# Kernel optimization log

Hardware: AMD Instinct MI355X
Metric: run time of the kernel (lower is better)

The kernel has to match this reference:

```python
import jax, jax.numpy as jnp
import numpy as np

TOP_K = 2  # num_experts_per_tok


def setup_inputs() -> dict:
    key = jax.random.key(0)
    ks = jax.random.split(key, 5)
    B, T, D, E, F = 2, 2048, 1024, 8, 2048
    scale_d = 1.0 / np.sqrt(D)
    scale_f = 1.0 / np.sqrt(F)
    return {
        "x": jax.random.normal(ks[0], (B, T, D), jnp.float32),
        "kernel_router_DE": jax.random.normal(ks[1], (D, E), jnp.float32) * scale_d,
        "kernel_gating_EDF": jax.random.normal(ks[2], (E, D, F), jnp.float32) * scale_d,
        "kernel_up_EDF": jax.random.normal(ks[3], (E, D, F), jnp.float32) * scale_d,
        "kernel_down_EFD": jax.random.normal(ks[4], (E, F, D), jnp.float32) * scale_f,
    }


def reference(x, kernel_router_DE, kernel_gating_EDF, kernel_up_EDF, kernel_down_EFD):
    E = kernel_router_DE.shape[-1]
    x = x.astype(jnp.float32)

    # --- Router: logits -> softmax -> top_k -> renormalize with softmax ---
    router_logits_BTE = jnp.einsum('BTD,DE->BTE', x, kernel_router_DE)
    probs_BTE = jax.nn.softmax(router_logits_BTE.astype(jnp.float32), axis=-1)
    weights_BTX, indices_BTX = jax.lax.top_k(probs_BTE, TOP_K)
    norm_weights_BTX = jax.nn.softmax(weights_BTX, axis=-1)

    # --- Scatter top-k weights back to dense per-expert weights ---
    one_hot_BTXE = jax.nn.one_hot(indices_BTX, num_classes=E, dtype=jnp.float32)
    full_weights_BTE = jnp.sum(one_hot_BTXE * norm_weights_BTX[..., None], axis=2)

    # --- Dense all-expert MLP (gating * up -> down), weighted combine ---
    gating_BTEF = jnp.einsum('BTD,EDF->BTEF', x, kernel_gating_EDF)
    fuse_BTEF = jax.nn.silu(gating_BTEF) * jnp.einsum('BTD,EDF->BTEF', x, kernel_up_EDF)
    down_BTED = jnp.einsum('BTEF,EFD->BTED', fuse_BTEF, kernel_down_EFD)
    out_BTD = jnp.einsum('BTED,BTE->BTD', down_BTED, full_weights_BTE)
    return out_BTD.astype(jnp.float32)
```

## Files before the change

### kernel.cpp

```cpp
#include <hip/hip_runtime.h>
#include <cstdint>

#define N_TOK 4096
#define DIM   1024
#define NEXP  8
#define FDIM  2048

typedef _Float16 f16_t;
typedef _Float16 f16x8 __attribute__((ext_vector_type(8)));
typedef float    f32x4 __attribute__((ext_vector_type(4)));

__device__ inline unsigned packh(float a, float b) {
    union { f16_t h[2]; unsigned u; } p;
    p.h[0] = (f16_t)a; p.h[1] = (f16_t)b;
    return p.u;
}

__device__ inline void gl2lds16(const void* g, void* l) {
    __builtin_amdgcn_global_load_lds(
        (const __attribute__((address_space(1))) unsigned*)g,
        (__attribute__((address_space(3))) unsigned*)l, 16, 0, 0);
}

__global__ __launch_bounds__(256) void router_kernel(
    const float* __restrict__ x, const float* __restrict__ wr,
    float* __restrict__ topw, int* __restrict__ counts, int* __restrict__ bucket)
{
    __shared__ float r[NEXP][DIM];
    __shared__ int sIdx[32];
    int tid = threadIdx.x;
    for (int i = tid; i < DIM * NEXP / 4; i += 256) {
        float4 v = ((const float4*)wr)[i];
        int base = i * 4;
        r[(base + 0) & 7][(base + 0) >> 3] = v.x;
        r[(base + 1) & 7][(base + 1) >> 3] = v.y;
        r[(base + 2) & 7][(base + 2) >> 3] = v.z;
        r[(base + 3) & 7][(base + 3) >> 3] = v.w;
    }
    __syncthreads();
    int wave = tid >> 6, lane = tid & 63;
    int t0 = blockIdx.x * 16 + wave * 4;
    for (int tt = 0; tt < 4; ++tt) {
        int t = t0 + tt;
        float acc[NEXP];
#pragma unroll
        for (int e = 0; e < NEXP; e++) acc[e] = 0.f;
        const float* xr = x + (size_t)t * DIM;
#pragma unroll
        for (int k = 0; k < DIM / 64; k++) {
            int d = lane + k * 64;
            float xv = xr[d];
#pragma unroll
            for (int e = 0; e < NEXP; e++) acc[e] += xv * r[e][d];
        }
#pragma unroll
        for (int e = 0; e < NEXP; e++) {
#pragma unroll
            for (int off = 32; off > 0; off >>= 1)
                acc[e] += __shfl_xor(acc[e], off, 64);
        }
        if (lane == 0) {
            float mx = acc[0];
#pragma unroll
            for (int e = 1; e < NEXP; e++) mx = fmaxf(mx, acc[e]);
            float p[NEXP]; float s = 0.f;
#pragma unroll
            for (int e = 0; e < NEXP; e++) { p[e] = expf(acc[e] - mx); s += p[e]; }
            float inv = 1.f / s;
#pragma unroll
            for (int e = 0; e < NEXP; e++) p[e] *= inv;
            int i1 = 0; float p1 = p[0];
#pragma unroll
            for (int e = 1; e < NEXP; e++) if (p[e] > p1) { p1 = p[e]; i1 = e; }
            int i2 = -1; float p2 = -1.f;
#pragma unroll
            for (int e = 0; e < NEXP; e++) if (e != i1 && p[e] > p2) { p2 = p[e]; i2 = e; }
            float e2 = expf(p2 - p1);
            float w1 = 1.f / (1.f + e2);
            topw[t * 2 + 0] = w1;
            topw[t * 2 + 1] = e2 * w1;
            int j = (wave * 4 + tt) * 2;
            sIdx[j + 0] = i1;
            sIdx[j + 1] = i2;
        }
    }
    __syncthreads();
    if (tid < NEXP) {
        int cnt = 0;
#pragma unroll
        for (int j = 0; j < 32; j++) cnt += (sIdx[j] == tid) ? 1 : 0;
        if (cnt > 0) {
            int pos = atomicAdd(&counts[tid * 32], cnt);
#pragma unroll
            for (int j = 0; j < 32; j++)
                if (sIdx[j] == tid)
                    bucket[tid * N_TOK + pos++] = (blockIdx.x * 16 + (j >> 1)) * 2 + (j & 1);
        }
    }
}

__global__ __launch_bounds__(256) void xcast_kernel(const float* __restrict__ x, f16_t* __restrict__ xf)
{
    int i = blockIdx.x * 256 + threadIdx.x;
    float4 a = ((const float4*)x)[2 * i];
    float4 b = ((const float4*)x)[2 * i + 1];
    union { f16_t h[8]; uint4 u; } p;
    p.h[0] = (f16_t)a.x; p.h[1] = (f16_t)a.y; p.h[2] = (f16_t)a.z; p.h[3] = (f16_t)a.w;
    p.h[4] = (f16_t)b.x; p.h[5] = (f16_t)b.y; p.h[6] = (f16_t)b.z; p.h[7] = (f16_t)b.w;
    ((uint4*)xf)[i] = p.u;
}

__global__ __launch_bounds__(256) void transpose_cvt(
    const float* __restrict__ inA, const float* __restrict__ inB,
    f16_t* __restrict__ outA, f16_t* __restrict__ outB,
    int R, int C, int tiles_r, int nA)
{
    __shared__ unsigned sP[64][68];
    int m = blockIdx.y;
    const float* in; f16_t* out;
    if (m < nA) { in = inA + (size_t)m * DIM * FDIM; out = outA + (size_t)m * DIM * FDIM; }
    else        { in = inB + (size_t)(m - nA) * DIM * FDIM; out = outB + (size_t)(m - nA) * DIM * FDIM; }
    int tix = blockIdx.x;
    int rb = (tix % tiles_r) * 128;
    int cb = (tix / tiles_r) * 64;
    int t = threadIdx.x;
    int dp = t >> 2;
    int fc = (t & 3) * 16;
    const float* r0 = in + (size_t)(rb + 2 * dp) * C + cb + fc;
    const float* r1 = r0 + C;
#pragma unroll
    for (int j = 0; j < 16; j += 4) {
        float4 a = *(const float4*)(r0 + j);
        float4 b = *(const float4*)(r1 + j);
        sP[fc + j + 0][dp] = packh(a.x, b.x);
        sP[fc + j + 1][dp] = packh(a.y, b.y);
        sP[fc + j + 2][dp] = packh(a.z, b.z);
        sP[fc + j + 3][dp] = packh(a.w, b.w);
    }
    __syncthreads();
    int c = t >> 2;
    int rc = t & 3;
    uint4* dst = (uint4*)(out + (size_t)(cb + c) * R + rb + rc * 32);
    const unsigned* src = &sP[c][rc * 16];
#pragma unroll
    for (int j = 0; j < 4; j++)
        dst[j] = *(const uint4*)(src + j * 4);
}

__global__ __launch_bounds__(256) void gateup_kernel(
    const f16_t* __restrict__ xf,
    const f16_t* __restrict__ wgT, const f16_t* __restrict__ wuT,
    const int* __restrict__ counts, const int* __restrict__ bucket,
    f16_t* __restrict__ H)
{
    int e = blockIdx.z;
    int cnt = counts[e * 32];
    int m0 = blockIdx.y * 128;
    if (m0 >= cnt) return;
    int n0 = blockIdx.x * 64;

    __shared__ f16_t sA[128 * 32];
    __shared__ f16_t sBg[64 * 32];
    __shared__ f16_t sBu[64 * 32];
    __shared__ int sEnt[128];

    int tid = threadIdx.x;
    if (tid < 128) {
        int i = m0 + tid;
        sEnt[tid] = bucket[e * N_TOK + (i < cnt ? i : m0)];
    }
    __syncthreads();

    int wave = tid >> 6, lane = tid & 63;
    int q = ((lane & 3) - (lane >> 3)) & 3;
    int rA0 = wave * 32 + (lane >> 2);
    int rA1 = rA0 + 16;
    int rB  = wave * 16 + (lane >> 2);
    const f16_t* gA0 = xf + (size_t)(sEnt[rA0] >> 1) * DIM + q * 8;
    const f16_t* gA1 = xf + (size_t)(sEnt[rA1] >> 1) * DIM + q * 8;
    const f16_t* gBg = wgT + ((size_t)e * FDIM + n0 + rB) * DIM + q * 8;
    const f16_t* gBu = wuT + ((size_t)e * FDIM + n0 + rB) * DIM + q * 8;
    f16_t* lA0 = &sA[wave * 1024 + lane * 8];
    f16_t* lA1 = lA0 + 512;
    f16_t* lBg = &sBg[wave * 512 + lane * 8];
    f16_t* lBu = &sBu[wave * 512 + lane * 8];

    f32x4 accG[4][2], accU[4][2];
    f32x4 zero = {0.f, 0.f, 0.f, 0.f};
#pragma unroll
    for (int i = 0; i < 4; i++)
#pragma unroll
        for (int j = 0; j < 2; j++) { accG[i][j] = zero; accU[i][j] = zero; }

    int wm = (wave & 1) * 64, wn = (wave >> 1) * 32;
    int fm = lane & 15, quad = lane >> 4;
    int p8 = ((quad + (fm >> 1)) & 3) * 8;

    for (int k0 = 0; k0 < DIM; k0 += 32) {
        gl2lds16(gA0 + k0, lA0);
        gl2lds16(gA1 + k0, lA1);
        gl2lds16(gBg + k0, lBg);
        gl2lds16(gBu + k0, lBu);
        __syncthreads();
        f16x8 af[4], bg[2], bu[2];
#pragma unroll
        for (int mi = 0; mi < 4; mi++)
            af[mi] = *(const f16x8*)&sA[(wm + mi * 16 + fm) * 32 + p8];
#pragma unroll
        for (int ni = 0; ni < 2; ni++) {
            bg[ni] = *(const f16x8*)&sBg[(wn + ni * 16 + fm) * 32 + p8];
            bu[ni] = *(const f16x8*)&sBu[(wn + ni * 16 + fm) * 32 + p8];
        }
#pragma unroll
        for (int mi = 0; mi < 4; mi++)
#pragma unroll
            for (int ni = 0; ni < 2; ni++) {
                accG[mi][ni] = __builtin_amdgcn_mfma_f32_16x16x32_f16(af[mi], bg[ni], accG[mi][ni], 0, 0, 0);
                accU[mi][ni] = __builtin_amdgcn_mfma_f32_16x16x32_f16(af[mi], bu[ni], accU[mi][ni], 0, 0, 0);
            }
        __syncthreads();
    }
    int crow = quad * 4, ccol = fm;
#pragma unroll
    for (int mi = 0; mi < 4; mi++) {
#pragma unroll
        for (int i = 0; i < 4; i++) {
            int m = wm + mi * 16 + crow + i;
            if (m0 + m < cnt) {
                int ent = sEnt[m];
                f16_t* hr = H + (size_t)ent * FDIM + n0 + wn;
#pragma unroll
                for (int ni = 0; ni < 2; ni++) {
                    float g = accG[mi][ni][i], u = accU[mi][ni][i];
                    float h = (g / (1.f + __expf(-g))) * u;
                    hr[ni * 16 + ccol] = (f16_t)h;
                }
            }
        }
    }
}

__global__ __launch_bounds__(256) void down_kernel(
    const f16_t* __restrict__ H, const f16_t* __restrict__ wdT,
    const int* __restrict__ counts, const int* __restrict__ bucket,
    const float* __restrict__ topw, float* __restrict__ Y)
{
    int e = blockIdx.z;
    int cnt = counts[e * 32];
    int m0 = blockIdx.y * 128;
    if (m0 >= cnt) return;
    int n0 = blockIdx.x * 128;

    __shared__ f16_t sA[128 * 32];
    __shared__ f16_t sB[128 * 32];
    __shared__ int sEnt[128];

    int tid = threadIdx.x;
    if (tid < 128) {
        int i = m0 + tid;
        sEnt[tid] = bucket[e * N_TOK + (i < cnt ? i : m0)];
    }
    __syncthreads();

    int wave = tid >> 6, lane = tid & 63;
    int q = ((lane & 3) - (lane >> 3)) & 3;
    int r0 = wave * 32 + (lane >> 2);
    int r1 = r0 + 16;
    const f16_t* gA0 = H + (size_t)sEnt[r0] * FDIM + q * 8;
    const f16_t* gA1 = H + (size_t)sEnt[r1] * FDIM + q * 8;
    const f16_t* gB0 = wdT + ((size_t)e * DIM + n0 + r0) * FDIM + q * 8;
    const f16_t* gB1 = wdT + ((size_t)e * DIM + n0 + r1) * FDIM + q * 8;
    f16_t* lA0 = &sA[wave * 1024 + lane * 8];
    f16_t* lA1 = lA0 + 512;
    f16_t* lB0 = &sB[wave * 1024 + lane * 8];
    f16_t* lB1 = lB0 + 512;

    f32x4 acc[4][4];
    f32x4 zero = {0.f, 0.f, 0.f, 0.f};
#pragma unroll
    for (int i = 0; i < 4; i++)
#pragma unroll
        for (int j = 0; j < 4; j++) acc[i][j] = zero;

    int wm = (wave & 1) * 64, wn = (wave >> 1) * 64;
    int fm = lane & 15, quad = lane >> 4;
    int p8 = ((quad + (fm >> 1)) & 3) * 8;

    for (int k0 = 0; k0 < FDIM; k0 += 32) {
        gl2lds16(gA0 + k0, lA0);
        gl2lds16(gA1 + k0, lA1);
        gl2lds16(gB0 + k0, lB0);
        gl2lds16(gB1 + k0, lB1);
        __syncthreads();
        f16x8 af[4], bf[4];
#pragma unroll
        for (int mi = 0; mi < 4; mi++)
            af[mi] = *(const f16x8*)&sA[(wm + mi * 16 + fm) * 32 + p8];
#pragma unroll
        for (int ni = 0; ni < 4; ni++)
            bf[ni] = *(const f16x8*)&sB[(wn + ni * 16 + fm) * 32 + p8];
#pragma unroll
        for (int mi = 0; mi < 4; mi++)
#pragma unroll
            for (int ni = 0; ni < 4; ni++)
                acc[mi][ni] = __builtin_amdgcn_mfma_f32_16x16x32_f16(af[mi], bf[ni], acc[mi][ni], 0, 0, 0);
        __syncthreads();
    }
    int crow = quad * 4, ccol = fm;
#pragma unroll
    for (int mi = 0; mi < 4; mi++) {
#pragma unroll
        for (int i = 0; i < 4; i++) {
            int m = wm + mi * 16 + crow + i;
            if (m0 + m < cnt) {
                int ent = sEnt[m];
                float w = topw[ent];
                float* yr = Y + (size_t)ent * DIM + n0 + wn;
#pragma unroll
                for (int ni = 0; ni < 4; ni++)
                    yr[ni * 16 + ccol] = w * acc[mi][ni][i];
            }
        }
    }
}

__global__ __launch_bounds__(256) void combine_kernel(
    const float* __restrict__ Y, float* __restrict__ out)
{
    int i = blockIdx.x * 256 + threadIdx.x;
    int t = i >> 8;
    int c = i & 255;
    float4 a = ((const float4*)Y)[(size_t)(2 * t) * 256 + c];
    float4 b = ((const float4*)Y)[(size_t)(2 * t + 1) * 256 + c];
    float4 o;
    o.x = a.x + b.x; o.y = a.y + b.y; o.z = a.z + b.z; o.w = a.w + b.w;
    ((float4*)out)[i] = o;
}

extern "C" void kernel_launch(void* const* d_in, const int* in_sizes, int n_in,
                              void* d_out, int out_size, void* d_ws, size_t ws_size,
                              hipStream_t stream) {
    const float* x  = (const float*)d_in[0];
    const float* wr = (const float*)d_in[1];
    const float* wg = (const float*)d_in[2];
    const float* wu = (const float*)d_in[3];
    const float* wd = (const float*)d_in[4];
    float* out = (float*)d_out;
    char* ws = (char*)d_ws;
    const size_t MB = 1ull << 20;

    int*   counts = (int*)ws;
    int*   bucket = (int*)(ws + 1024);
    float* topw   = (float*)(ws + 160 * 1024);
    f16_t* xf     = (f16_t*)(ws + 1 * MB);
    f16_t* wgT    = (f16_t*)(ws + 9 * MB);
    f16_t* wuT    = (f16_t*)(ws + 41 * MB);
    f16_t* H      = (f16_t*)(ws + 73 * MB);
    f16_t* wdT    = (f16_t*)(ws + 1 * MB);
    float* Y      = (float*)(ws + 33 * MB);

    hipMemsetAsync(counts, 0, 1024, stream);
    router_kernel<<<256, 256, 0, stream>>>(x, wr, topw, counts, bucket);
    xcast_kernel<<<2048, 256, 0, stream>>>(x, xf);
    transpose_cvt<<<dim3(256, 16), 256, 0, stream>>>(wg, wu, wgT, wuT, DIM, FDIM, DIM / 128, NEXP);
    gateup_kernel<<<dim3(FDIM / 64, 32, NEXP), 256, 0, stream>>>(xf, wgT, wuT, counts, bucket, H);
    transpose_cvt<<<dim3(256, 8), 256, 0, stream>>>(wd, wd, wdT, wdT, FDIM, DIM, FDIM / 128, NEXP);
    down_kernel<<<dim3(DIM / 128, 32, NEXP), 256, 0, stream>>>(H, wdT, counts, bucket, topw, Y);
    combine_kernel<<<4096, 256, 0, stream>>>(Y, out);
}
```

Baseline: 413.7 us.

## Fuse prep kernels, convert down weights in-loop, combine via atomics

New measurement: 444.7 us. 7.5% more time.

```diff
diff --git a/kernel.cpp b/kernel.cpp
--- a/kernel.cpp
+++ b/kernel.cpp
@@ -22,24 +22,75 @@
         (__attribute__((address_space(3))) unsigned*)l, 16, 0, 0);
 }
 
-__global__ __launch_bounds__(256) void router_kernel(
+__global__ __launch_bounds__(256) void prep_kernel(
     const float* __restrict__ x, const float* __restrict__ wr,
-    float* __restrict__ topw, int* __restrict__ counts, int* __restrict__ bucket)
+    float* __restrict__ topw, int* __restrict__ counts, int* __restrict__ bucket,
+    f16_t* __restrict__ xf,
+    const float* __restrict__ wg, const float* __restrict__ wu,
+    f16_t* __restrict__ wgT, f16_t* __restrict__ wuT)
 {
-    __shared__ float r[NEXP][DIM];
+    __shared__ union { float r[NEXP][DIM]; unsigned sP[64][68]; } sm;
     __shared__ int sIdx[32];
     int tid = threadIdx.x;
+
+    if (blockIdx.x >= 256) {
+        int b2 = blockIdx.x - 256;
+        int m = b2 >> 8;
+        int tix = b2 & 255;
+        const float* in; f16_t* out;
+        if (m < 8) { in = wg + (size_t)m * DIM * FDIM;       out = wgT + (size_t)m * DIM * FDIM; }
+        else       { in = wu + (size_t)(m - 8) * DIM * FDIM; out = wuT + (size_t)(m - 8) * DIM * FDIM; }
+        int rb = (tix & 7) * 128;
+        int cb = (tix >> 3) * 64;
+        int dp = tid >> 2;
+        int fc = (tid & 3) * 16;
+        const float* r0 = in + (size_t)(rb + 2 * dp) * FDIM + cb + fc;
+        const float* r1 = r0 + FDIM;
+#pragma unroll
+        for (int j = 0; j < 16; j += 4) {
+            float4 a = *(const float4*)(r0 + j);
+            float4 b = *(const float4*)(r1 + j);
+            sm.sP[fc + j + 0][dp] = packh(a.x, b.x);
+            sm.sP[fc + j + 1][dp] = packh(a.y, b.y);
+            sm.sP[fc + j + 2][dp] = packh(a.z, b.z);
+            sm.sP[fc + j + 3][dp] = packh(a.w, b.w);
+        }
+        __syncthreads();
+        int c = tid >> 2;
+        int rc = tid & 3;
+        uint4* dst = (uint4*)(out + (size_t)(cb + c) * DIM + rb + rc * 32);
+        const unsigned* src = &sm.sP[c][rc * 16];
+#pragma unroll
+        for (int j = 0; j < 4; j++)
+            dst[j] = *(const uint4*)(src + j * 4);
+        return;
+    }
+
+    int blk = blockIdx.x;
+    {
+        const float* xblk = x + (size_t)blk * 16 * DIM;
+        f16_t* xfblk = xf + (size_t)blk * 16 * DIM;
+#pragma unroll
+        for (int i = tid; i < 16 * DIM / 8; i += 256) {
+            float4 a = ((const float4*)xblk)[2 * i];
+            float4 b = ((const float4*)xblk)[2 * i + 1];
+            union { f16_t h[8]; uint4 u; } pk;
+            pk.h[0] = (f16_t)a.x; pk.h[1] = (f16_t)a.y; pk.h[2] = (f16_t)a.z; pk.h[3] = (f16_t)a.w;
+            pk.h[4] = (f16_t)b.x; pk.h[5] = (f16_t)b.y; pk.h[6] = (f16_t)b.z; pk.h[7] = (f16_t)b.w;
+            ((uint4*)xfblk)[i] = pk.u;
+        }
+    }
     for (int i = tid; i < DIM * NEXP / 4; i += 256) {
         float4 v = ((const float4*)wr)[i];
         int base = i * 4;
-        r[(base + 0) & 7][(base + 0) >> 3] = v.x;
-        r[(base + 1) & 7][(base + 1) >> 3] = v.y;
-        r[(base + 2) & 7][(base + 2) >> 3] = v.z;
-        r[(base + 3) & 7][(base + 3) >> 3] = v.w;
+        sm.r[(base + 0) & 7][(base + 0) >> 3] = v.x;
+        sm.r[(base + 1) & 7][(base + 1) >> 3] = v.y;
+        sm.r[(base + 2) & 7][(base + 2) >> 3] = v.z;
+        sm.r[(base + 3) & 7][(base + 3) >> 3] = v.w;
     }
     __syncthreads();
     int wave = tid >> 6, lane = tid & 63;
-    int t0 = blockIdx.x * 16 + wave * 4;
+    int t0 = blk * 16 + wave * 4;
     for (int tt = 0; tt < 4; ++tt) {
         int t = t0 + tt;
         float acc[NEXP];
@@ -51,7 +102,7 @@
             int d = lane + k * 64;
             float xv = xr[d];
 #pragma unroll
-            for (int e = 0; e < NEXP; e++) acc[e] += xv * r[e][d];
+            for (int e = 0; e < NEXP; e++) acc[e] += xv * sm.r[e][d];
         }
 #pragma unroll
         for (int e = 0; e < NEXP; e++) {
@@ -94,57 +145,9 @@
 #pragma unroll
             for (int j = 0; j < 32; j++)
                 if (sIdx[j] == tid)
-                    bucket[tid * N_TOK + pos++] = (blockIdx.x * 16 + (j >> 1)) * 2 + (j & 1);
-        }
-    }
-}
-
-__global__ __launch_bounds__(256) void xcast_kernel(const float* __restrict__ x, f16_t* __restrict__ xf)
-{
-    int i = blockIdx.x * 256 + threadIdx.x;
-    float4 a = ((const float4*)x)[2 * i];
-    float4 b = ((const float4*)x)[2 * i + 1];
-    union { f16_t h[8]; uint4 u; } p;
-    p.h[0] = (f16_t)a.x; p.h[1] = (f16_t)a.y; p.h[2] = (f16_t)a.z; p.h[3] = (f16_t)a.w;
-    p.h[4] = (f16_t)b.x; p.h[5] = (f16_t)b.y; p.h[6] = (f16_t)b.z; p.h[7] = (f16_t)b.w;
-    ((uint4*)xf)[i] = p.u;
-}
-
-__global__ __launch_bounds__(256) void transpose_cvt(
-    const float* __restrict__ inA, const float* __restrict__ inB,
-    f16_t* __restrict__ outA, f16_t* __restrict__ outB,
-    int R, int C, int tiles_r, int nA)
-{
-    __shared__ unsigned sP[64][68];
-    int m = blockIdx.y;
-    const float* in; f16_t* out;
-    if (m < nA) { in = inA + (size_t)m * DIM * FDIM; out = outA + (size_t)m * DIM * FDIM; }
-    else        { in = inB + (size_t)(m - nA) * DIM * FDIM; out = outB + (size_t)(m - nA) * DIM * FDIM; }
-    int tix = blockIdx.x;
-    int rb = (tix % tiles_r) * 128;
-    int cb = (tix / tiles_r) * 64;
-    int t = threadIdx.x;
-    int dp = t >> 2;
-    int fc = (t & 3) * 16;
-    const float* r0 = in + (size_t)(rb + 2 * dp) * C + cb + fc;
-    const float* r1 = r0 + C;
-#pragma unroll
-    for (int j = 0; j < 16; j += 4) {
-        float4 a = *(const float4*)(r0 + j);
-        float4 b = *(const float4*)(r1 + j);
-        sP[fc + j + 0][dp] = packh(a.x, b.x);
-        sP[fc + j + 1][dp] = packh(a.y, b.y);
-        sP[fc + j + 2][dp] = packh(a.z, b.z);
-        sP[fc + j + 3][dp] = packh(a.w, b.w);
-    }
-    __syncthreads();
-    int c = t >> 2;
-    int rc = t & 3;
-    uint4* dst = (uint4*)(out + (size_t)(cb + c) * R + rb + rc * 32);
-    const unsigned* src = &sP[c][rc * 16];
-#pragma unroll
-    for (int j = 0; j < 4; j++)
-        dst[j] = *(const uint4*)(src + j * 4);
+                    bucket[tid * N_TOK + pos++] = (blk * 16 + (j >> 1)) * 2 + (j & 1);
+        }
+    }
 }
 
 __global__ __launch_bounds__(256) void gateup_kernel(
@@ -153,11 +156,13 @@
     const int* __restrict__ counts, const int* __restrict__ bucket,
     f16_t* __restrict__ H)
 {
-    int e = blockIdx.z;
+    int flat = blockIdx.x;
+    int e = flat & 7;
+    int idx = flat >> 3;
+    int m0 = (idx & 31) * 128;
+    int n0 = (idx >> 5) * 64;
     int cnt = counts[e * 32];
-    int m0 = blockIdx.y * 128;
     if (m0 >= cnt) return;
-    int n0 = blockIdx.x * 64;
 
     __shared__ f16_t sA[128 * 32];
     __shared__ f16_t sBg[64 * 32];
@@ -241,15 +246,17 @@
 }
 
 __global__ __launch_bounds__(256) void down_kernel(
-    const f16_t* __restrict__ H, const f16_t* __restrict__ wdT,
+    const f16_t* __restrict__ H, const float* __restrict__ wd,
     const int* __restrict__ counts, const int* __restrict__ bucket,
-    const float* __restrict__ topw, float* __restrict__ Y)
+    const float* __restrict__ topw, float* __restrict__ out)
 {
-    int e = blockIdx.z;
+    int flat = blockIdx.x;
+    int e = flat & 7;
+    int idx = flat >> 3;
+    int m0 = (idx & 31) * 128;
+    int n0 = (idx >> 5) * 128;
     int cnt = counts[e * 32];
-    int m0 = blockIdx.y * 128;
     if (m0 >= cnt) return;
-    int n0 = blockIdx.x * 128;
 
     __shared__ f16_t sA[128 * 32];
     __shared__ f16_t sB[128 * 32];
@@ -268,12 +275,27 @@
     int r1 = r0 + 16;
     const f16_t* gA0 = H + (size_t)sEnt[r0] * FDIM + q * 8;
     const f16_t* gA1 = H + (size_t)sEnt[r1] * FDIM + q * 8;
-    const f16_t* gB0 = wdT + ((size_t)e * DIM + n0 + r0) * FDIM + q * 8;
-    const f16_t* gB1 = wdT + ((size_t)e * DIM + n0 + r1) * FDIM + q * 8;
     f16_t* lA0 = &sA[wave * 1024 + lane * 8];
     f16_t* lA1 = lA0 + 512;
-    f16_t* lB0 = &sB[wave * 1024 + lane * 8];
-    f16_t* lB1 = lB0 + 512;
+
+    int fp = tid & 7;
+    int dq = tid >> 3;
+    int fp2 = fp * 2;
+    const float* wde = wd + (size_t)e * FDIM * DIM + n0 + dq * 4;
+    int o2 = (fp & 3) * 2;
+    int g0 = (fp >> 2);
+    int g1 = 2 + (fp >> 2);
+    int cA = ((g0 ^ (dq & 3)) * 8) + o2;
+    int cB = ((g1 ^ (dq & 3)) * 8) + o2;
+    int rowb = dq * 4;
+
+    float4 pb0, pb1, pb2, pb3;
+#define LOADB(K0) {                                                             \
+        const float* rr = wde + (size_t)((K0) + fp2) * DIM;                     \
+        pb0 = *(const float4*)rr;                                               \
+        pb1 = *(const float4*)(rr + DIM);                                       \
+        pb2 = *(const float4*)(rr + 16 * DIM);                                  \
+        pb3 = *(const float4*)(rr + 17 * DIM); }
 
     f32x4 acc[4][4];
     f32x4 zero = {0.f, 0.f, 0.f, 0.f};
@@ -286,19 +308,29 @@
     int fm = lane & 15, quad = lane >> 4;
     int p8 = ((quad + (fm >> 1)) & 3) * 8;
 
+    LOADB(0);
     for (int k0 = 0; k0 < FDIM; k0 += 32) {
         gl2lds16(gA0 + k0, lA0);
         gl2lds16(gA1 + k0, lA1);
-        gl2lds16(gB0 + k0, lB0);
-        gl2lds16(gB1 + k0, lB1);
-        __syncthreads();
+        *(unsigned*)&sB[(rowb + 0) * 32 + cA] = packh(pb0.x, pb1.x);
+        *(unsigned*)&sB[(rowb + 1) * 32 + cA] = packh(pb0.y, pb1.y);
+        *(unsigned*)&sB[(rowb + 2) * 32 + cA] = packh(pb0.z, pb1.z);
+        *(unsigned*)&sB[(rowb + 3) * 32 + cA] = packh(pb0.w, pb1.w);
+        *(unsigned*)&sB[(rowb + 0) * 32 + cB] = packh(pb2.x, pb3.x);
+        *(unsigned*)&sB[(rowb + 1) * 32 + cB] = packh(pb2.y, pb3.y);
+        *(unsigned*)&sB[(rowb + 2) * 32 + cB] = packh(pb2.z, pb3.z);
+        *(unsigned*)&sB[(rowb + 3) * 32 + cB] = packh(pb2.w, pb3.w);
+        __syncthreads();
+        if (k0 + 32 < FDIM) LOADB(k0 + 32);
         f16x8 af[4], bf[4];
 #pragma unroll
         for (int mi = 0; mi < 4; mi++)
             af[mi] = *(const f16x8*)&sA[(wm + mi * 16 + fm) * 32 + p8];
 #pragma unroll
-        for (int ni = 0; ni < 4; ni++)
-            bf[ni] = *(const f16x8*)&sB[(wn + ni * 16 + fm) * 32 + p8];
+        for (int ni = 0; ni < 4; ni++) {
+            int row = wn + ni * 16 + fm;
+            bf[ni] = *(const f16x8*)&sB[row * 32 + (quad ^ ((row >> 2) & 3)) * 8];
+        }
 #pragma unroll
         for (int mi = 0; mi < 4; mi++)
 #pragma unroll
@@ -306,6 +338,8 @@
                 acc[mi][ni] = __builtin_amdgcn_mfma_f32_16x16x32_f16(af[mi], bf[ni], acc[mi][ni], 0, 0, 0);
         __syncthreads();
     }
+#undef LOADB
+
     int crow = quad * 4, ccol = fm;
 #pragma unroll
     for (int mi = 0; mi < 4; mi++) {
@@ -315,26 +349,13 @@
             if (m0 + m < cnt) {
                 int ent = sEnt[m];
                 float w = topw[ent];
-                float* yr = Y + (size_t)ent * DIM + n0 + wn;
+                float* orow = out + (size_t)(ent >> 1) * DIM + n0 + wn;
 #pragma unroll
                 for (int ni = 0; ni < 4; ni++)
-                    yr[ni * 16 + ccol] = w * acc[mi][ni][i];
+                    atomicAdd(&orow[ni * 16 + ccol], w * acc[mi][ni][i]);
             }
         }
     }
-}
-
-__global__ __launch_bounds__(256) void combine_kernel(
-    const float* __restrict__ Y, float* __restrict__ out)
-{
-    int i = blockIdx.x * 256 + threadIdx.x;
-    int t = i >> 8;
-    int c = i & 255;
-    float4 a = ((const float4*)Y)[(size_t)(2 * t) * 256 + c];
-    float4 b = ((const float4*)Y)[(size_t)(2 * t + 1) * 256 + c];
-    float4 o;
-    o.x = a.x + b.x; o.y = a.y + b.y; o.z = a.z + b.z; o.w = a.w + b.w;
-    ((float4*)out)[i] = o;
 }
 
 extern "C" void kernel_launch(void* const* d_in, const int* in_sizes, int n_in,
@@ -356,15 +377,10 @@
     f16_t* wgT    = (f16_t*)(ws + 9 * MB);
     f16_t* wuT    = (f16_t*)(ws + 41 * MB);
     f16_t* H      = (f16_t*)(ws + 73 * MB);
-    f16_t* wdT    = (f16_t*)(ws + 1 * MB);
-    float* Y      = (float*)(ws + 33 * MB);
 
     hipMemsetAsync(counts, 0, 1024, stream);
-    router_kernel<<<256, 256, 0, stream>>>(x, wr, topw, counts, bucket);
-    xcast_kernel<<<2048, 256, 0, stream>>>(x, xf);
-    transpose_cvt<<<dim3(256, 16), 256, 0, stream>>>(wg, wu, wgT, wuT, DIM, FDIM, DIM / 128, NEXP);
-    gateup_kernel<<<dim3(FDIM / 64, 32, NEXP), 256, 0, stream>>>(xf, wgT, wuT, counts, bucket, H);
-    transpose_cvt<<<dim3(256, 8), 256, 0, stream>>>(wd, wd, wdT, wdT, FDIM, DIM, FDIM / 128, NEXP);
-    down_kernel<<<dim3(DIM / 128, 32, NEXP), 256, 0, stream>>>(H, wdT, counts, bucket, topw, Y);
-    combine_kernel<<<4096, 256, 0, stream>>>(Y, out);
-}
+    hipMemsetAsync(out, 0, out_size, stream);
+    prep_kernel<<<4352, 256, 0, stream>>>(x, wr, topw, counts, bucket, xf, wg, wu, wgT, wuT);
+    gateup_kernel<<<8192, 256, 0, stream>>>(xf, wgT, wuT, counts, bucket, H);
+    down_kernel<<<2048, 256, 0, stream>>>(H, wd, counts, bucket, topw, out);
+}
```
